# Kernel optimization log

Measured on AMD Instinct MI355X. Metric: run time of the kernel, lower is better.

The kernel has to match this reference:

```python
import jax, jax.numpy as jnp
import numpy as np

DIM = 2048
NUM_HEADS = 16
HEAD_DIM = DIM // NUM_HEADS  # 128
SEQ_LEN = 2048
ROPE_THETA = 10000.0


def _rope_tables(T, head_dim, dtype=jnp.float32):
    inv_freq = 1.0 / (ROPE_THETA ** (jnp.arange(0, head_dim, 2, dtype=jnp.float32) / head_dim))
    t = jnp.arange(T, dtype=jnp.float32)
    freqs = jnp.outer(t, inv_freq)  # [T, head_dim//2]
    return jnp.cos(freqs).astype(dtype), jnp.sin(freqs).astype(dtype)


def setup_inputs() -> dict:
    key = jax.random.key(0)
    ks = jax.random.split(key, 9)
    s = 1.0 / jnp.sqrt(DIM)
    x = jax.random.normal(ks[0], (SEQ_LEN, DIM), dtype=jnp.float32)
    wq = jax.random.uniform(ks[1], (DIM, DIM), minval=-s, maxval=s, dtype=jnp.float32)
    wk = jax.random.uniform(ks[2], (DIM, DIM), minval=-s, maxval=s, dtype=jnp.float32)
    wv = jax.random.uniform(ks[3], (DIM, DIM), minval=-s, maxval=s, dtype=jnp.float32)
    wp = jax.random.uniform(ks[4], (DIM, DIM), minval=-s, maxval=s, dtype=jnp.float32)
    bq = jax.random.uniform(ks[5], (DIM,), minval=-s, maxval=s, dtype=jnp.float32)
    bk = jax.random.uniform(ks[6], (DIM,), minval=-s, maxval=s, dtype=jnp.float32)
    bv = jax.random.uniform(ks[7], (DIM,), minval=-s, maxval=s, dtype=jnp.float32)
    bp = jax.random.uniform(ks[8], (DIM,), minval=-s, maxval=s, dtype=jnp.float32)
    cos, sin = _rope_tables(SEQ_LEN, HEAD_DIM)
    return {"x": x, "wq": wq, "bq": bq, "wk": wk, "bk": bk, "wv": wv, "bv": bv,
            "wp": wp, "bp": bp, "cos": cos, "sin": sin}


def _apply_rope(t, cos, sin):
    # t: [T, H, D]; cos/sin: [T, D//2]
    T, H, D = t.shape
    tr = t.reshape(T, H, D // 2, 2)
    r, i = tr[..., 0], tr[..., 1]
    c = cos[:, None, :]
    s = sin[:, None, :]
    out = jnp.stack([r * c - i * s, r * s + i * c], axis=-1)
    return out.reshape(T, H, D)


def reference(x, wq, bq, wk, bk, wv, bv, wp, bp, cos, sin):
    T, C = x.shape
    H, D = NUM_HEADS, C // NUM_HEADS
    q = (x @ wq.T + bq).reshape(T, H, D)
    k = (x @ wk.T + bk).reshape(T, H, D)
    v = (x @ wv.T + bv).reshape(T, H, D)
    q = _apply_rope(q, cos, sin)
    k = _apply_rope(k, cos, sin)
    # scores: [H, T, T]; NOTE: source scales by full dim C, not head_dim
    attn = jnp.einsum('thd,shd->hts', q, k) * (C ** -0.5)
    mask = jnp.tril(jnp.ones((T, T), dtype=bool))
    attn = jnp.where(mask[None], attn, -jnp.inf)
    attn = jax.nn.softmax(attn, axis=-1)
    out = jnp.einsum('hts,shd->thd', attn, v).reshape(T, C)
    return out @ wp.T + bp
```

## Files before the change

### kernel.cpp

```cpp
#include <hip/hip_runtime.h>
#include <math.h>

typedef __attribute__((ext_vector_type(8))) short  bf16x8;
typedef __attribute__((ext_vector_type(4))) float  f32x4;
typedef __attribute__((ext_vector_type(8))) ushort u16x8;

#define SEQ   2048
#define CDIM  2048
#define NHEAD 16
#define DHEAD 128
#define SCALE 0.02209708691207961f
#define LOG2E 1.4426950408889634f

__device__ __forceinline__ ushort f2bf(float f) {
    uint u = __float_as_uint(f);
    u += 0x7FFFu + ((u >> 16) & 1u);
    return (ushort)(u >> 16);
}
__device__ __forceinline__ float bf2f(ushort h) {
    return __uint_as_float(((uint)h) << 16);
}

#define GLOAD16(gsrc, ldst)                                                  \
    __builtin_amdgcn_global_load_lds(                                        \
        (const __attribute__((address_space(1))) void*)(gsrc),               \
        (__attribute__((address_space(3))) void*)(ldst), 16, 0, 0)

__global__ __launch_bounds__(256) void f2bf_kernel(const float* __restrict__ src,
                                                   ushort* __restrict__ dst, int n8)
{
    const int i = blockIdx.x * 256 + threadIdx.x;
    if (i >= n8) return;
    const float4 a = ((const float4*)src)[i * 2];
    const float4 b = ((const float4*)src)[i * 2 + 1];
    u16x8 o;
    o[0] = f2bf(a.x); o[1] = f2bf(a.y); o[2] = f2bf(a.z); o[3] = f2bf(a.w);
    o[4] = f2bf(b.x); o[5] = f2bf(b.y); o[6] = f2bf(b.z); o[7] = f2bf(b.w);
    *(u16x8*)&dst[(size_t)i * 8] = o;
}

template <bool OUT_BF16>
__global__ __launch_bounds__(256) void gemm_nt_mfma(const ushort* __restrict__ A,
                                                    const ushort* __restrict__ B,
                                                    const float* __restrict__ bias,
                                                    void* __restrict__ outp)
{
    __shared__ ushort As[128 * 32];
    __shared__ ushort Bs[128 * 32];
    const int tid  = threadIdx.x;
    const int lane = tid & 63, wid = tid >> 6;
    const int wr = wid >> 1, wc = wid & 1;
    const int l4 = lane >> 4, l15 = lane & 15;
    const int m0 = blockIdx.y * 128, n0 = blockIdx.x * 128;

    f32x4 acc[4][4];
    #pragma unroll
    for (int i = 0; i < 4; ++i)
        #pragma unroll
        for (int j = 0; j < 4; ++j) acc[i][j] = 0.f;

    const int srow = wid * 32 + (lane >> 2);
    const int scol = (lane & 3) * 8;

    for (int k0 = 0; k0 < CDIM; k0 += 32) {
        __syncthreads();
        GLOAD16(&A[(size_t)(m0 + srow)      * CDIM + k0 + scol], (char*)As + wid * 2048);
        GLOAD16(&A[(size_t)(m0 + srow + 16) * CDIM + k0 + scol], (char*)As + wid * 2048 + 1024);
        GLOAD16(&B[(size_t)(n0 + srow)      * CDIM + k0 + scol], (char*)Bs + wid * 2048);
        GLOAD16(&B[(size_t)(n0 + srow + 16) * CDIM + k0 + scol], (char*)Bs + wid * 2048 + 1024);
        __syncthreads();

        bf16x8 af[4], bfr[4];
        #pragma unroll
        for (int f = 0; f < 4; ++f) {
            af[f]  = *(const bf16x8*)&As[(wr * 64 + f * 16 + l15) * 32 + l4 * 8];
            bfr[f] = *(const bf16x8*)&Bs[(wc * 64 + f * 16 + l15) * 32 + l4 * 8];
        }
        #pragma unroll
        for (int i = 0; i < 4; ++i)
            #pragma unroll
            for (int j = 0; j < 4; ++j)
                acc[i][j] = __builtin_amdgcn_mfma_f32_16x16x32_bf16(af[i], bfr[j], acc[i][j], 0, 0, 0);
    }

    float bn[4];
    #pragma unroll
    for (int j = 0; j < 4; ++j) bn[j] = bias[n0 + wc * 64 + j * 16 + l15];

    #pragma unroll
    for (int i = 0; i < 4; ++i) {
        #pragma unroll
        for (int j = 0; j < 4; ++j) {
            const int n = n0 + wc * 64 + j * 16 + l15;
            #pragma unroll
            for (int r = 0; r < 4; ++r) {
                const int m = m0 + wr * 64 + i * 16 + l4 * 4 + r;
                const float v = acc[i][j][r] + bn[j];
                if (OUT_BF16) ((ushort*)outp)[(size_t)m * CDIM + n] = f2bf(v);
                else          ((float*)outp)[(size_t)m * CDIM + n] = v;
            }
        }
    }
}

__global__ __launch_bounds__(256) void rope_bf16(ushort* __restrict__ q, ushort* __restrict__ k,
                                                 const float* __restrict__ cosT,
                                                 const float* __restrict__ sinT)
{
    const int idx = blockIdx.x * 256 + threadIdx.x;
    ushort* buf = blockIdx.y ? k : q;
    const int base = idx * 8;
    const int t   = base >> 11;
    const int fi0 = (base & 127) >> 1;
    const float4 c4 = *(const float4*)&cosT[t * 64 + fi0];
    const float4 s4 = *(const float4*)&sinT[t * 64 + fi0];
    const float c[4] = {c4.x, c4.y, c4.z, c4.w};
    const float s[4] = {s4.x, s4.y, s4.z, s4.w};
    u16x8 v = *(const u16x8*)&buf[base];
    u16x8 o;
    #pragma unroll
    for (int p = 0; p < 4; ++p) {
        const float r  = bf2f(v[2 * p]);
        const float im = bf2f(v[2 * p + 1]);
        o[2 * p]     = f2bf(r * c[p] - im * s[p]);
        o[2 * p + 1] = f2bf(r * s[p] + im * c[p]);
    }
    *(u16x8*)&buf[base] = o;
}

__global__ __launch_bounds__(256) void flash_attn_mfma(const ushort* __restrict__ qb,
                                                       const ushort* __restrict__ kb,
                                                       const ushort* __restrict__ vb,
                                                       ushort* __restrict__ ao)
{
    __shared__ ushort Ks[64 * 136];
    __shared__ ushort Vt[128 * 72];
    __shared__ float  S_lds[64 * 68];
    __shared__ ushort Ps[64 * 72];
    __shared__ float  rowM[64], rowL[64], rowF[64];

    const int tid  = threadIdx.x;
    const int lane = tid & 63, wid = tid >> 6;
    const int wr = wid >> 1, wc = wid & 1;
    const int l4 = lane >> 4, l15 = lane & 15;
    const int h = blockIdx.y, qt = blockIdx.x;
    const int q0 = qt * 64;

    if (tid < 64) { rowM[tid] = -INFINITY; rowL[tid] = 0.f; }

    bf16x8 qf[2][4];
    #pragma unroll
    for (int fm = 0; fm < 2; ++fm)
        #pragma unroll
        for (int ks = 0; ks < 4; ++ks) {
            const int row = q0 + wr * 32 + fm * 16 + l15;
            const int col = h * DHEAD + ks * 32 + l4 * 8;
            qf[fm][ks] = *(const bf16x8*)&qb[(size_t)row * CDIM + col];
        }

    f32x4 acc_o[2][4];
    #pragma unroll
    for (int fm = 0; fm < 2; ++fm)
        #pragma unroll
        for (int fn = 0; fn < 4; ++fn) acc_o[fm][fn] = 0.f;

    for (int kt = 0; kt <= qt; ++kt) {
        __syncthreads();

        #pragma unroll
        for (int i2 = 0; i2 < 4; ++i2) {
            const int r  = (tid >> 4) + i2 * 16;
            const int c8 = (tid & 15) * 8;
            *(u16x8*)&Ks[r * 136 + c8] =
                *(const u16x8*)&kb[(size_t)(kt * 64 + r) * CDIM + h * DHEAD + c8];
        }
        #pragma unroll
        for (int i2 = 0; i2 < 4; ++i2) {
            const int kv = (tid >> 4) + i2 * 16;
            const int d0 = (tid & 15) * 8;
            u16x8 vv = *(const u16x8*)&vb[(size_t)(kt * 64 + kv) * CDIM + h * DHEAD + d0];
            #pragma unroll
            for (int e = 0; e < 8; ++e) {
                const int d = d0 + e;
                const uint byteoff = (uint)(d * 144 + kv * 2) ^ ((((uint)d >> 3) & 7u) << 4);
                *(ushort*)((char*)Vt + byteoff) = vv[e];
            }
        }
        __syncthreads();

        f32x4 sacc[2][2];
        #pragma unroll
        for (int fm = 0; fm < 2; ++fm)
            #pragma unroll
            for (int fn = 0; fn < 2; ++fn) sacc[fm][fn] = 0.f;
        #pragma unroll
        for (int ks = 0; ks < 4; ++ks) {
            bf16x8 kf[2];
            #pragma unroll
            for (int fn = 0; fn < 2; ++fn)
                kf[fn] = *(const bf16x8*)&Ks[(wc * 32 + fn * 16 + l15) * 136 + ks * 32 + l4 * 8];
            #pragma unroll
            for (int fm = 0; fm < 2; ++fm)
                #pragma unroll
                for (int fn = 0; fn < 2; ++fn)
                    sacc[fm][fn] = __builtin_amdgcn_mfma_f32_16x16x32_bf16(qf[fm][ks], kf[fn], sacc[fm][fn], 0, 0, 0);
        }
        #pragma unroll
        for (int fm = 0; fm < 2; ++fm)
            #pragma unroll
            for (int fn = 0; fn < 2; ++fn)
                #pragma unroll
                for (int r = 0; r < 4; ++r) {
                    const int srow = wr * 32 + fm * 16 + l4 * 4 + r;
                    const int scol = wc * 32 + fn * 16 + l15;
                    float sv = sacc[fm][fn][r] * SCALE;
                    if (kt == qt && scol > srow) sv = -INFINITY;
                    S_lds[srow * 68 + scol] = sv;
                }
        __syncthreads();

        {
            const int srow = tid >> 2;
            const int c0   = (tid & 3) * 16;
            float vals[16];
            #pragma unroll
            for (int c = 0; c < 16; ++c) vals[c] = S_lds[srow * 68 + c0 + c];
            float mt = vals[0];
            #pragma unroll
            for (int c = 1; c < 16; ++c) mt = fmaxf(mt, vals[c]);
            mt = fmaxf(mt, __shfl_xor(mt, 1));
            mt = fmaxf(mt, __shfl_xor(mt, 2));
            const float mold = rowM[srow];
            const float mnew = fmaxf(mold, mt);
            float sum = 0.f;
            ushort pb[16];
            #pragma unroll
            for (int c = 0; c < 16; ++c) {
                const float p = exp2f((vals[c] - mnew) * LOG2E);
                sum += p;
                pb[c] = f2bf(p);
            }
            sum += __shfl_xor(sum, 1);
            sum += __shfl_xor(sum, 2);
            u16x8 w0, w1;
            #pragma unroll
            for (int c = 0; c < 8; ++c) { w0[c] = pb[c]; w1[c] = pb[c + 8]; }
            *(u16x8*)&Ps[srow * 72 + c0]     = w0;
            *(u16x8*)&Ps[srow * 72 + c0 + 8] = w1;
            if ((tid & 3) == 0) {
                const float fac = exp2f((mold - mnew) * LOG2E);
                rowF[srow] = fac;
                rowL[srow] = rowL[srow] * fac + sum;
                rowM[srow] = mnew;
            }
        }
        __syncthreads();

        float frv[2][4];
        #pragma unroll
        for (int fm = 0; fm < 2; ++fm)
            #pragma unroll
            for (int r = 0; r < 4; ++r)
                frv[fm][r] = rowF[wr * 32 + fm * 16 + l4 * 4 + r];
        #pragma unroll
        for (int fm = 0; fm < 2; ++fm)
            #pragma unroll
            for (int fn = 0; fn < 4; ++fn)
                #pragma unroll
                for (int r = 0; r < 4; ++r) acc_o[fm][fn][r] *= frv[fm][r];

        #pragma unroll
        for (int ks = 0; ks < 2; ++ks) {
            bf16x8 pa[2];
            #pragma unroll
            for (int fm = 0; fm < 2; ++fm)
                pa[fm] = *(const bf16x8*)&Ps[(wr * 32 + fm * 16 + l15) * 72 + ks * 32 + l4 * 8];
            #pragma unroll
            for (int fn = 0; fn < 4; ++fn) {
                const int n = wc * 64 + fn * 16 + l15;
                const uint byteoff = (uint)(n * 144 + ks * 64 + l4 * 16) ^ ((((uint)n >> 3) & 7u) << 4);
                bf16x8 vf = *(const bf16x8*)((const char*)Vt + byteoff);
                #pragma unroll
                for (int fm = 0; fm < 2; ++fm)
                    acc_o[fm][fn] = __builtin_amdgcn_mfma_f32_16x16x32_bf16(pa[fm], vf, acc_o[fm][fn], 0, 0, 0);
            }
        }
    }

    #pragma unroll
    for (int fm = 0; fm < 2; ++fm) {
        #pragma unroll
        for (int r = 0; r < 4; ++r) {
            const int lrow = wr * 32 + fm * 16 + l4 * 4 + r;
            const float invl = 1.f / rowL[lrow];
            #pragma unroll
            for (int fn = 0; fn < 4; ++fn) {
                const int gcol = h * DHEAD + wc * 64 + fn * 16 + l15;
                ao[(size_t)(q0 + lrow) * CDIM + gcol] = f2bf(acc_o[fm][fn][r] * invl);
            }
        }
    }
}

extern "C" void kernel_launch(void* const* d_in, const int* in_sizes, int n_in,
                              void* d_out, int out_size, void* d_ws, size_t ws_size,
                              hipStream_t stream) {
    const float* x    = (const float*)d_in[0];
    const float* wq   = (const float*)d_in[1];
    const float* bq   = (const float*)d_in[2];
    const float* wk   = (const float*)d_in[3];
    const float* bk   = (const float*)d_in[4];
    const float* wv   = (const float*)d_in[5];
    const float* bv   = (const float*)d_in[6];
    const float* wp   = (const float*)d_in[7];
    const float* bp   = (const float*)d_in[8];
    const float* cosT = (const float*)d_in[9];
    const float* sinT = (const float*)d_in[10];
    float* out = (float*)d_out;

    const size_t mat = (size_t)SEQ * CDIM;
    ushort* xb  = (ushort*)d_ws;
    ushort* wb  = xb  + mat;
    ushort* qbb = wb  + mat;
    ushort* kbb = qbb + mat;
    ushort* vbb = kbb + mat;
    ushort* aob = vbb + mat;

    const int n8 = (int)(mat / 8);
    const dim3 cgrid(n8 / 256);
    const dim3 ggrid(16, 16);

    f2bf_kernel<<<cgrid, 256, 0, stream>>>(x, xb, n8);

    f2bf_kernel<<<cgrid, 256, 0, stream>>>(wq, wb, n8);
    gemm_nt_mfma<true><<<ggrid, 256, 0, stream>>>(xb, wb, bq, (void*)qbb);
    f2bf_kernel<<<cgrid, 256, 0, stream>>>(wk, wb, n8);
    gemm_nt_mfma<true><<<ggrid, 256, 0, stream>>>(xb, wb, bk, (void*)kbb);
    f2bf_kernel<<<cgrid, 256, 0, stream>>>(wv, wb, n8);
    gemm_nt_mfma<true><<<ggrid, 256, 0, stream>>>(xb, wb, bv, (void*)vbb);

    rope_bf16<<<dim3(SEQ * CDIM / 8 / 256, 2), 256, 0, stream>>>(qbb, kbb, cosT, sinT);

    flash_attn_mfma<<<dim3(SEQ / 64, NHEAD), 256, 0, stream>>>(qbb, kbb, vbb, aob);

    f2bf_kernel<<<cgrid, 256, 0, stream>>>(wp, wb, n8);
    gemm_nt_mfma<false><<<ggrid, 256, 0, stream>>>(aob, wb, bp, d_out);

    (void)out; (void)in_sizes; (void)n_in; (void)out_size; (void)ws_size;
}
```

Baseline: 405.7 us.

## Batch QKV projections into one launch, emit transposed V, reverse attention tile order

Converts the three QKV weight matrices in one launch and runs all three projection GEMMs as a single 3D grid (768 blocks instead of three 256-block launches), which improves GPU fill. The V projection writes its output transposed, so the attention kernel can load V^T tiles with vector copies instead of scattered per-element swizzled LDS stores. The attention grid is also reversed so the heaviest causal tiles are scheduled first. Costs include separate workspace buffers for each weight, strided 8-byte stores in the V epilogue, and dropping the LDS swizzle on the V^T reads, which may add bank conflicts.

```diff
diff --git a/kernel.cpp b/kernel.cpp
--- a/kernel.cpp
+++ b/kernel.cpp
@@ -4,6 +4,7 @@
 typedef __attribute__((ext_vector_type(8))) short  bf16x8;
 typedef __attribute__((ext_vector_type(4))) float  f32x4;
 typedef __attribute__((ext_vector_type(8))) ushort u16x8;
+typedef __attribute__((ext_vector_type(4))) ushort u16x4;
 
 #define SEQ   2048
 #define CDIM  2048
@@ -39,11 +40,29 @@
     *(u16x8*)&dst[(size_t)i * 8] = o;
 }
 
-template <bool OUT_BF16>
-__global__ __launch_bounds__(256) void gemm_nt_mfma(const ushort* __restrict__ A,
-                                                    const ushort* __restrict__ B,
-                                                    const float* __restrict__ bias,
-                                                    void* __restrict__ outp)
+__global__ __launch_bounds__(256) void f2bf3_kernel(const float* __restrict__ s0,
+                                                    const float* __restrict__ s1,
+                                                    const float* __restrict__ s2,
+                                                    ushort* __restrict__ d0,
+                                                    ushort* __restrict__ d1,
+                                                    ushort* __restrict__ d2)
+{
+    const int z = blockIdx.y;
+    const float* src = z == 0 ? s0 : z == 1 ? s1 : s2;
+    ushort*      dst = z == 0 ? d0 : z == 1 ? d1 : d2;
+    const int i = blockIdx.x * 256 + threadIdx.x;
+    const float4 a = ((const float4*)src)[i * 2];
+    const float4 b = ((const float4*)src)[i * 2 + 1];
+    u16x8 o;
+    o[0] = f2bf(a.x); o[1] = f2bf(a.y); o[2] = f2bf(a.z); o[3] = f2bf(a.w);
+    o[4] = f2bf(b.x); o[5] = f2bf(b.y); o[6] = f2bf(b.z); o[7] = f2bf(b.w);
+    *(u16x8*)&dst[(size_t)i * 8] = o;
+}
+
+__global__ __launch_bounds__(256) void gemm_nt_mfma_f32(const ushort* __restrict__ A,
+                                                        const ushort* __restrict__ B,
+                                                        const float* __restrict__ bias,
+                                                        float* __restrict__ outp)
 {
     __shared__ ushort As[128 * 32];
     __shared__ ushort Bs[128 * 32];
@@ -88,18 +107,100 @@
     for (int j = 0; j < 4; ++j) bn[j] = bias[n0 + wc * 64 + j * 16 + l15];
 
     #pragma unroll
-    for (int i = 0; i < 4; ++i) {
+    for (int i = 0; i < 4; ++i)
         #pragma unroll
         for (int j = 0; j < 4; ++j) {
             const int n = n0 + wc * 64 + j * 16 + l15;
             #pragma unroll
             for (int r = 0; r < 4; ++r) {
                 const int m = m0 + wr * 64 + i * 16 + l4 * 4 + r;
-                const float v = acc[i][j][r] + bn[j];
-                if (OUT_BF16) ((ushort*)outp)[(size_t)m * CDIM + n] = f2bf(v);
-                else          ((float*)outp)[(size_t)m * CDIM + n] = v;
-            }
-        }
+                outp[(size_t)m * CDIM + n] = acc[i][j][r] + bn[j];
+            }
+        }
+}
+
+__global__ __launch_bounds__(256) void gemm_qkv(const ushort* __restrict__ A,
+                                                const ushort* __restrict__ W0,
+                                                const ushort* __restrict__ W1,
+                                                const ushort* __restrict__ W2,
+                                                const float* __restrict__ b0,
+                                                const float* __restrict__ b1,
+                                                const float* __restrict__ b2,
+                                                ushort* __restrict__ o0,
+                                                ushort* __restrict__ o1,
+                                                ushort* __restrict__ o2)
+{
+    __shared__ ushort As[128 * 32];
+    __shared__ ushort Bs[128 * 32];
+    const int z = blockIdx.z;
+    const ushort* B    = z == 0 ? W0 : z == 1 ? W1 : W2;
+    const float*  bias = z == 0 ? b0 : z == 1 ? b1 : b2;
+
+    const int tid  = threadIdx.x;
+    const int lane = tid & 63, wid = tid >> 6;
+    const int wr = wid >> 1, wc = wid & 1;
+    const int l4 = lane >> 4, l15 = lane & 15;
+    const int m0 = blockIdx.y * 128, n0 = blockIdx.x * 128;
+
+    f32x4 acc[4][4];
+    #pragma unroll
+    for (int i = 0; i < 4; ++i)
+        #pragma unroll
+        for (int j = 0; j < 4; ++j) acc[i][j] = 0.f;
+
+    const int srow = wid * 32 + (lane >> 2);
+    const int scol = (lane & 3) * 8;
+
+    for (int k0 = 0; k0 < CDIM; k0 += 32) {
+        __syncthreads();
+        GLOAD16(&A[(size_t)(m0 + srow)      * CDIM + k0 + scol], (char*)As + wid * 2048);
+        GLOAD16(&A[(size_t)(m0 + srow + 16) * CDIM + k0 + scol], (char*)As + wid * 2048 + 1024);
+        GLOAD16(&B[(size_t)(n0 + srow)      * CDIM + k0 + scol], (char*)Bs + wid * 2048);
+        GLOAD16(&B[(size_t)(n0 + srow + 16) * CDIM + k0 + scol], (char*)Bs + wid * 2048 + 1024);
+        __syncthreads();
+
+        bf16x8 af[4], bfr[4];
+        #pragma unroll
+        for (int f = 0; f < 4; ++f) {
+            af[f]  = *(const bf16x8*)&As[(wr * 64 + f * 16 + l15) * 32 + l4 * 8];
+            bfr[f] = *(const bf16x8*)&Bs[(wc * 64 + f * 16 + l15) * 32 + l4 * 8];
+        }
+        #pragma unroll
+        for (int i = 0; i < 4; ++i)
+            #pragma unroll
+            for (int j = 0; j < 4; ++j)
+                acc[i][j] = __builtin_amdgcn_mfma_f32_16x16x32_bf16(af[i], bfr[j], acc[i][j], 0, 0, 0);
+    }
+
+    float bn[4];
+    #pragma unroll
+    for (int j = 0; j < 4; ++j) bn[j] = bias[n0 + wc * 64 + j * 16 + l15];
+
+    if (z == 2) {
+        #pragma unroll
+        for (int i = 0; i < 4; ++i)
+            #pragma unroll
+            for (int j = 0; j < 4; ++j) {
+                const int n = n0 + wc * 64 + j * 16 + l15;
+                const int mb = m0 + wr * 64 + i * 16 + l4 * 4;
+                u16x4 pk;
+                #pragma unroll
+                for (int r = 0; r < 4; ++r) pk[r] = f2bf(acc[i][j][r] + bn[j]);
+                *(u16x4*)&o2[(size_t)n * SEQ + mb] = pk;
+            }
+    } else {
+        ushort* outp = z == 0 ? o0 : o1;
+        #pragma unroll
+        for (int i = 0; i < 4; ++i)
+            #pragma unroll
+            for (int j = 0; j < 4; ++j) {
+                const int n = n0 + wc * 64 + j * 16 + l15;
+                #pragma unroll
+                for (int r = 0; r < 4; ++r) {
+                    const int m = m0 + wr * 64 + i * 16 + l4 * 4 + r;
+                    outp[(size_t)m * CDIM + n] = f2bf(acc[i][j][r] + bn[j]);
+                }
+            }
     }
 }
 
@@ -130,11 +231,11 @@
 
 __global__ __launch_bounds__(256) void flash_attn_mfma(const ushort* __restrict__ qb,
                                                        const ushort* __restrict__ kb,
-                                                       const ushort* __restrict__ vb,
+                                                       const ushort* __restrict__ vT,
                                                        ushort* __restrict__ ao)
 {
     __shared__ ushort Ks[64 * 136];
-    __shared__ ushort Vt[128 * 72];
+    __shared__ ushort VTs[128 * 72];
     __shared__ float  S_lds[64 * 68];
     __shared__ ushort Ps[64 * 72];
     __shared__ float  rowM[64], rowL[64], rowF[64];
@@ -143,7 +244,8 @@
     const int lane = tid & 63, wid = tid >> 6;
     const int wr = wid >> 1, wc = wid & 1;
     const int l4 = lane >> 4, l15 = lane & 15;
-    const int h = blockIdx.y, qt = blockIdx.x;
+    const int h = blockIdx.y;
+    const int qt = gridDim.x - 1 - blockIdx.x;
     const int q0 = qt * 64;
 
     if (tid < 64) { rowM[tid] = -INFINITY; rowL[tid] = 0.f; }
@@ -176,15 +278,10 @@
         }
         #pragma unroll
         for (int i2 = 0; i2 < 4; ++i2) {
-            const int kv = (tid >> 4) + i2 * 16;
-            const int d0 = (tid & 15) * 8;
-            u16x8 vv = *(const u16x8*)&vb[(size_t)(kt * 64 + kv) * CDIM + h * DHEAD + d0];
-            #pragma unroll
-            for (int e = 0; e < 8; ++e) {
-                const int d = d0 + e;
-                const uint byteoff = (uint)(d * 144 + kv * 2) ^ ((((uint)d >> 3) & 7u) << 4);
-                *(ushort*)((char*)Vt + byteoff) = vv[e];
-            }
+            const int r  = (tid >> 3) + i2 * 32;
+            const int c8 = (tid & 7) * 8;
+            *(u16x8*)&VTs[r * 72 + c8] =
+                *(const u16x8*)&vT[(size_t)(h * DHEAD + r) * SEQ + kt * 64 + c8];
         }
         __syncthreads();
 
@@ -277,9 +374,7 @@
                 pa[fm] = *(const bf16x8*)&Ps[(wr * 32 + fm * 16 + l15) * 72 + ks * 32 + l4 * 8];
             #pragma unroll
             for (int fn = 0; fn < 4; ++fn) {
-                const int n = wc * 64 + fn * 16 + l15;
-                const uint byteoff = (uint)(n * 144 + ks * 64 + l4 * 16) ^ ((((uint)n >> 3) & 7u) << 4);
-                bf16x8 vf = *(const bf16x8*)((const char*)Vt + byteoff);
+                bf16x8 vf = *(const bf16x8*)&VTs[(wc * 64 + fn * 16 + l15) * 72 + ks * 32 + l4 * 8];
                 #pragma unroll
                 for (int fm = 0; fm < 2; ++fm)
                     acc_o[fm][fn] = __builtin_amdgcn_mfma_f32_16x16x32_bf16(pa[fm], vf, acc_o[fm][fn], 0, 0, 0);
@@ -288,7 +383,7 @@
     }
 
     #pragma unroll
-    for (int fm = 0; fm < 2; ++fm) {
+    for (int fm = 0; fm < 2; ++fm)
         #pragma unroll
         for (int r = 0; r < 4; ++r) {
             const int lrow = wr * 32 + fm * 16 + l4 * 4 + r;
@@ -299,7 +394,6 @@
                 ao[(size_t)(q0 + lrow) * CDIM + gcol] = f2bf(acc_o[fm][fn][r] * invl);
             }
         }
-    }
 }
 
 extern "C" void kernel_launch(void* const* d_in, const int* in_sizes, int n_in,
@@ -316,35 +410,32 @@
     const float* bp   = (const float*)d_in[8];
     const float* cosT = (const float*)d_in[9];
     const float* sinT = (const float*)d_in[10];
-    float* out = (float*)d_out;
 
     const size_t mat = (size_t)SEQ * CDIM;
     ushort* xb  = (ushort*)d_ws;
-    ushort* wb  = xb  + mat;
-    ushort* qbb = wb  + mat;
+    ushort* w0  = xb  + mat;
+    ushort* w1  = w0  + mat;
+    ushort* w2  = w1  + mat;
+    ushort* qbb = w2  + mat;
     ushort* kbb = qbb + mat;
-    ushort* vbb = kbb + mat;
-    ushort* aob = vbb + mat;
+    ushort* vTb = kbb + mat;
+    ushort* aob = w0;
 
     const int n8 = (int)(mat / 8);
     const dim3 cgrid(n8 / 256);
-    const dim3 ggrid(16, 16);
 
     f2bf_kernel<<<cgrid, 256, 0, stream>>>(x, xb, n8);
-
-    f2bf_kernel<<<cgrid, 256, 0, stream>>>(wq, wb, n8);
-    gemm_nt_mfma<true><<<ggrid, 256, 0, stream>>>(xb, wb, bq, (void*)qbb);
-    f2bf_kernel<<<cgrid, 256, 0, stream>>>(wk, wb, n8);
-    gemm_nt_mfma<true><<<ggrid, 256, 0, stream>>>(xb, wb, bk, (void*)kbb);
-    f2bf_kernel<<<cgrid, 256, 0, stream>>>(wv, wb, n8);
-    gemm_nt_mfma<true><<<ggrid, 256, 0, stream>>>(xb, wb, bv, (void*)vbb);
+    f2bf3_kernel<<<dim3(n8 / 256, 3), 256, 0, stream>>>(wq, wk, wv, w0, w1, w2);
+
+    gemm_qkv<<<dim3(16, 16, 3), 256, 0, stream>>>(xb, w0, w1, w2, bq, bk, bv,
+                                                  qbb, kbb, vTb);
 
     rope_bf16<<<dim3(SEQ * CDIM / 8 / 256, 2), 256, 0, stream>>>(qbb, kbb, cosT, sinT);
 
-    flash_attn_mfma<<<dim3(SEQ / 64, NHEAD), 256, 0, stream>>>(qbb, kbb, vbb, aob);
-
-    f2bf_kernel<<<cgrid, 256, 0, stream>>>(wp, wb, n8);
-    gemm_nt_mfma<false><<<ggrid, 256, 0, stream>>>(aob, wb, bp, d_out);
-
-    (void)out; (void)in_sizes; (void)n_in; (void)out_size; (void)ws_size;
-}
+    flash_attn_mfma<<<dim3(SEQ / 64, NHEAD), 256, 0, stream>>>(qbb, kbb, vTb, aob);
+
+    f2bf_kernel<<<cgrid, 256, 0, stream>>>(wp, w1, n8);
+    gemm_nt_mfma_f32<<<dim3(16, 16), 256, 0, stream>>>(aob, w1, bp, (float*)d_out);
+
+    (void)in_sizes; (void)n_in; (void)out_size; (void)ws_size;
+}
```

Measured after the change: 351.5 us. 13.4% less time.
